# Kernel optimization log

Hardware: AMD Instinct MI355X
Metric: run time of the kernel (lower is better)

The kernel has to match this reference:

```python
import jax, jax.numpy as jnp
import numpy as np

NEG_INF = -1e6  # d2l masked_softmax mask value

def setup_inputs() -> dict:
    key = jax.random.key(0)
    ks = jax.random.split(key, 6)
    B, Lq, Lk, dq, dv, H = 8, 256, 512, 256, 256, 64
    return {
        "queries": jax.random.normal(ks[0], (B, Lq, dq), jnp.float32),
        "keys": jax.random.normal(ks[1], (B, Lk, dq), jnp.float32),
        "values": jax.random.normal(ks[2], (B, Lk, dv), jnp.float32),
        "valid_lens": jax.random.randint(ks[3], (B,), 0, Lk),
        "W_q": jax.random.normal(ks[4], (H, dq), jnp.float32) * (dq ** -0.5),
        "W_k": jax.random.normal(ks[5], (H, dq), jnp.float32) * (dq ** -0.5),
        "w_v": jax.random.normal(jax.random.fold_in(key, 7), (H,), jnp.float32) * (H ** -0.5),
    }

def reference(queries, keys, values, valid_lens, W_q, W_k, w_v):
    # Project: [B,Lq,H], [B,Lk,H]
    q = jnp.einsum('bqd,hd->bqh', queries, W_q)
    k = jnp.einsum('bkd,hd->bkh', keys, W_k)
    # Broadcast-add + tanh: [B,Lq,Lk,H]
    features = jnp.tanh(q[:, :, None, :] + k[:, None, :, :])
    # Scalar projection -> scores [B,Lq,Lk]
    scores = jnp.einsum('bqkh,h->bqk', features, w_v)
    # masked_softmax over last axis with per-batch valid_lens
    Lk = keys.shape[1]
    mask = jnp.arange(Lk)[None, None, :] < valid_lens[:, None, None]
    scores = jnp.where(mask, scores, NEG_INF)
    attn = jax.nn.softmax(scores, axis=-1)
    # dropout p=0 (inference) -> identity; bmm with values
    return jnp.einsum('bqk,bkv->bqv', attn, values)
```

## Files before the change

### kernel.cpp

```cpp
#include <hip/hip_runtime.h>
#include <hip/hip_bf16.h>
#include <hip/hip_fp16.h>
#include <stdint.h>

#define NB 8
#define LQ 256
#define LK 512
#define NH 64
#define SCALE 2.8853900817779268f
#define L2E 1.4426950408889634f

#define QP_OFF   0
#define KP_OFF   131072
#define VBF_OFF  393216
#define PML_OFF  917504

extern "C" __device__ float __ocml_exp2_f32(float);
static __device__ __forceinline__ float fexp2(float x) {
#if __has_builtin(__builtin_amdgcn_exp2f)
  return __builtin_amdgcn_exp2f(x);
#else
  return __ocml_exp2_f32(x);
#endif
}
static __device__ __forceinline__ float frcp(float x) {
  return __builtin_amdgcn_rcpf(x);
}
static __device__ __forceinline__ uint16_t f2bf(float f) {
  uint32_t u = __float_as_uint(f);
  uint32_t r = (u + 0x7FFFu + ((u >> 16) & 1u)) >> 16;
  return (uint16_t)r;
}

typedef const __attribute__((address_space(1))) void* gas_ptr;
typedef __attribute__((address_space(3))) void* las_ptr;
static __device__ __forceinline__ void gload16(const void* g, void* l) {
  __builtin_amdgcn_global_load_lds((gas_ptr)g, (las_ptr)l, 16, 0, 0);
}

__global__ __launch_bounds__(256) void proj_kernel(
    const float* __restrict__ queries, const float* __restrict__ keys,
    const float* __restrict__ values,
    const float* __restrict__ Wq, const float* __restrict__ Wk,
    float* __restrict__ qp, float* __restrict__ kp, uint16_t* __restrict__ vbf)
{
  __shared__ float Wt[256][36];
  const int blk = blockIdx.x;
  const int t = threadIdx.x;

  if (blk >= 384) {
    int base = (blk - 384) * 16384 + t * 4;
#pragma unroll
    for (int it = 0; it < 16; ++it) {
      int idx = base + it * 1024;
      float4 v = *(const float4*)(values + idx);
      uint32_t lo = (uint32_t)f2bf(v.x) | ((uint32_t)f2bf(v.y) << 16);
      uint32_t hi = (uint32_t)f2bf(v.z) | ((uint32_t)f2bf(v.w) << 16);
      uint2 pk = {lo, hi};
      *(uint2*)(vbf + idx) = pk;
    }
    return;
  }

  const bool isQ = (blk < 128);
  const int sub = isQ ? blk : (blk - 128);
  const int tile = sub >> 1;
  const int hh = (sub & 1) * 32;
  const int rowbase = tile * 32;
  const float* __restrict__ X = isQ ? queries : keys;
  const float* __restrict__ W = isQ ? Wq : Wk;
  float* __restrict__ P = isQ ? qp : kp;

#pragma unroll 4
  for (int it = 0; it < 32; ++it) {
    Wt[t][it] = W[(hh + it) * 256 + t];
  }
  __syncthreads();

  const int ty = t >> 4;
  const int tx = t & 15;
  float acc[2][2];
  acc[0][0] = acc[0][1] = acc[1][0] = acc[1][1] = 0.f;

  const float* xr0 = X + (rowbase + ty * 2 + 0) * 256;
  const float* xr1 = X + (rowbase + ty * 2 + 1) * 256;

#pragma unroll 4
  for (int d4 = 0; d4 < 64; ++d4) {
    int d = d4 * 4;
    float4 x0 = *(const float4*)(xr0 + d);
    float4 x1 = *(const float4*)(xr1 + d);
    float2 w0 = *(float2*)&Wt[d + 0][tx * 2];
    float2 w1 = *(float2*)&Wt[d + 1][tx * 2];
    float2 w2 = *(float2*)&Wt[d + 2][tx * 2];
    float2 w3 = *(float2*)&Wt[d + 3][tx * 2];
#define STEP(XC, WD) \
    acc[0][0] = fmaf(x0.XC, WD.x, acc[0][0]); acc[0][1] = fmaf(x0.XC, WD.y, acc[0][1]); \
    acc[1][0] = fmaf(x1.XC, WD.x, acc[1][0]); acc[1][1] = fmaf(x1.XC, WD.y, acc[1][1]);
    STEP(x, w0) STEP(y, w1) STEP(z, w2) STEP(w, w3)
#undef STEP
  }

#pragma unroll
  for (int i = 0; i < 2; ++i) {
    int row = rowbase + ty * 2 + i;
#pragma unroll
    for (int j = 0; j < 2; ++j) {
      int h = hh + tx * 2 + j;
      P[row * 64 + h] = acc[i][j] * SCALE;
    }
  }
}

__global__ __launch_bounds__(256) void attn_kernel(
    const float* __restrict__ qp, const float* __restrict__ kp,
    const uint16_t* __restrict__ vbf, const float* __restrict__ w_v,
    const int* __restrict__ valid_lens, float* __restrict__ out,
    float* __restrict__ pml, __half* __restrict__ pacc, int nsplit)
{
  __shared__ float kTs[2][32][64];
  __shared__ uint16_t Vs[2][32][256];
  __shared__ float q_s[4][2][64];
  __shared__ float w_s[64];
  __shared__ float p_s[4][2][32];

  const int t = threadIdx.x;
  const int lane = t & 63;
  const int w = t >> 6;
  const int r2 = lane >> 5;
  const int kj = lane & 31;
  const int wg = blockIdx.x;
  const int b = wg & 7;
  const int qg = (wg >> 3) & 31;
  const int kh = wg >> 8;
  const int row = b * LQ + qg * 8 + w * 2 + r2;

  const int vl = valid_lens[b];
  const int n = (vl > 0) ? vl : LK;
  const int span = LK / nsplit;
  const int kstart = kh * span;
  int cnt = n - kstart;
  if (cnt > span) cnt = span;
  const int ntiles = (cnt > 0) ? ((cnt + 31) >> 5) : 0;

  if (ntiles == 0) {
    if (kj == 0) {
      pml[(row * nsplit + kh) * 2 + 0] = -1e30f;
      pml[(row * nsplit + kh) * 2 + 1] = 0.f;
    }
    return;
  }

  {
    const float2* qsrc = (const float2*)(qp + (size_t)(b * LQ + qg * 8) * 64);
    ((float2*)q_s)[t] = qsrc[t];
    if (t < 64) w_s[t] = w_v[t];
  }

  float W1 = 0.f;
#pragma unroll
  for (int g = 0; g < 16; ++g) {
    float4 wf = *(const float4*)(w_v + g * 4);
    W1 += (wf.x + wf.y) + (wf.z + wf.w);
  }

  const float* kpb = kp + (size_t)(b * LK) * 64;
  const char* vbc = (const char*)(vbf + (size_t)b * LK * 256);

#define STAGE(BUF, K0) do { \
    int i0 = w * 2; \
    int kjr0 = i0 * 4 + (lane >> 4); \
    int cph = lane & 15; \
    gload16(kpb + (size_t)((K0) + kjr0) * 64 + (cph ^ (kjr0 & 7)) * 4, \
            &kTs[BUF][i0 * 4][0]); \
    int kjr1 = kjr0 + 4; \
    gload16(kpb + (size_t)((K0) + kjr1) * 64 + (cph ^ (kjr1 & 7)) * 4, \
            &kTs[BUF][i0 * 4 + 4][0]); \
    const char* vsrc = vbc + (size_t)(K0) * 512 + (size_t)w * 4096 + lane * 16; \
    gload16(vsrc + 0 * 1024, &Vs[BUF][w * 8 + 0][0]); \
    gload16(vsrc + 1 * 1024, &Vs[BUF][w * 8 + 2][0]); \
    gload16(vsrc + 2 * 1024, &Vs[BUF][w * 8 + 4][0]); \
    gload16(vsrc + 3 * 1024, &Vs[BUF][w * 8 + 6][0]); \
  } while (0)

  float m = -1e30f, l = 0.f;
  float acc[8];
#pragma unroll
  for (int i = 0; i < 8; ++i) acc[i] = 0.f;

  STAGE(0, kstart);
  __syncthreads();

  for (int tt = 0; tt < ntiles; ++tt) {
    const int cur = tt & 1;
    const int k0 = kstart + tt * 32;
    if (tt + 1 < ntiles) STAGE(cur ^ 1, k0 + 32);

    float r0 = 0.f, r1 = 0.f, r2a = 0.f, r3 = 0.f;
#pragma unroll
    for (int g = 0; g < 16; ++g) {
      float4 kf = *(const float4*)&kTs[cur][kj][((g ^ (kj & 7)) << 2)];
      float4 qf = *(const float4*)&q_s[w][r2][g * 4];
      float4 wf = *(const float4*)&w_s[g * 4];
      r0  = fmaf(wf.x, frcp(1.f + fexp2(qf.x + kf.x)), r0);
      r1  = fmaf(wf.y, frcp(1.f + fexp2(qf.y + kf.y)), r1);
      r2a = fmaf(wf.z, frcp(1.f + fexp2(qf.z + kf.z)), r2a);
      r3  = fmaf(wf.w, frcp(1.f + fexp2(qf.w + kf.w)), r3);
    }
    float racc = (r0 + r1) + (r2a + r3);

    float score;
    int kg = k0 + kj;
    if (vl == 0)      score = 0.f;
    else if (kg < n)  score = fmaf(-2.f, racc, W1);
    else              score = -1e30f;

    float mt = score;
#pragma unroll
    for (int s = 16; s; s >>= 1) mt = fmaxf(mt, __shfl_xor(mt, s, 64));
    float mnew = fmaxf(m, mt);
    float alpha = fexp2((m - mnew) * L2E);
    float p = fexp2((score - mnew) * L2E);
    m = mnew;
    float S = p;
#pragma unroll
    for (int s = 16; s; s >>= 1) S += __shfl_xor(S, s, 64);
    l = l * alpha + S;
    p_s[w][r2][kj] = p;

#pragma unroll
    for (int i = 0; i < 8; ++i) acc[i] *= alpha;
#pragma unroll
    for (int kj4 = 0; kj4 < 8; ++kj4) {
      float4 pf = *(const float4*)&p_s[w][r2][kj4 * 4];
#pragma unroll
      for (int jj = 0; jj < 4; ++jj) {
        int kk = kj4 * 4 + jj;
        uint4 vv = *(const uint4*)&Vs[cur][kk][kj * 8];
        float pj = (jj == 0) ? pf.x : (jj == 1) ? pf.y : (jj == 2) ? pf.z : pf.w;
        float f0 = __uint_as_float(vv.x << 16);
        float f1 = __uint_as_float(vv.x & 0xFFFF0000u);
        float f2 = __uint_as_float(vv.y << 16);
        float f3 = __uint_as_float(vv.y & 0xFFFF0000u);
        float f4 = __uint_as_float(vv.z << 16);
        float f5 = __uint_as_float(vv.z & 0xFFFF0000u);
        float f6 = __uint_as_float(vv.w << 16);
        float f7 = __uint_as_float(vv.w & 0xFFFF0000u);
        acc[0] = fmaf(pj, f0, acc[0]);
        acc[1] = fmaf(pj, f1, acc[1]);
        acc[2] = fmaf(pj, f2, acc[2]);
        acc[3] = fmaf(pj, f3, acc[3]);
        acc[4] = fmaf(pj, f4, acc[4]);
        acc[5] = fmaf(pj, f5, acc[5]);
        acc[6] = fmaf(pj, f6, acc[6]);
        acc[7] = fmaf(pj, f7, acc[7]);
      }
    }
    __syncthreads();
  }
#undef STAGE

  if (nsplit == 1) {
    float inv = 1.f / l;
    float4 o0 = {acc[0] * inv, acc[1] * inv, acc[2] * inv, acc[3] * inv};
    float4 o1 = {acc[4] * inv, acc[5] * inv, acc[6] * inv, acc[7] * inv};
    float* op = out + (size_t)row * 256 + kj * 8;
    *(float4*)(op + 0) = o0;
    *(float4*)(op + 4) = o1;
  } else {
    if (kj == 0) {
      pml[(row * nsplit + kh) * 2 + 0] = m;
      pml[(row * nsplit + kh) * 2 + 1] = l;
    }
    __half2 h0 = __floats2half2_rn(acc[0], acc[1]);
    __half2 h1 = __floats2half2_rn(acc[2], acc[3]);
    __half2 h2 = __floats2half2_rn(acc[4], acc[5]);
    __half2 h3 = __floats2half2_rn(acc[6], acc[7]);
    uint4 pk = {*(uint32_t*)&h0, *(uint32_t*)&h1, *(uint32_t*)&h2, *(uint32_t*)&h3};
    *(uint4*)(pacc + ((size_t)(row * nsplit + kh)) * 256 + kj * 8) = pk;
  }
}

__global__ __launch_bounds__(256) void merge_kernel(
    const float* __restrict__ pml, const __half* __restrict__ pacc,
    float* __restrict__ out, int nsplit)
{
  const int t = threadIdx.x;
  const int row = blockIdx.x * 8 + (t >> 5);
  const int d8 = t & 31;

  float ms = -1e30f;
  for (int kh = 0; kh < nsplit; ++kh)
    ms = fmaxf(ms, pml[(row * nsplit + kh) * 2]);

  float L = 0.f;
  float o[8];
#pragma unroll
  for (int i = 0; i < 8; ++i) o[i] = 0.f;

  for (int kh = 0; kh < nsplit; ++kh) {
    float mk = pml[(row * nsplit + kh) * 2 + 0];
    float lk = pml[(row * nsplit + kh) * 2 + 1];
    if (lk > 0.f) {
      float e = fexp2((mk - ms) * L2E);
      L += e * lk;
      uint4 pk = *(const uint4*)(pacc + ((size_t)(row * nsplit + kh)) * 256 + d8 * 8);
      __half2 h0 = *(__half2*)&pk.x, h1 = *(__half2*)&pk.y;
      __half2 h2 = *(__half2*)&pk.z, h3 = *(__half2*)&pk.w;
      float2 f0 = __half22float2(h0), f1 = __half22float2(h1);
      float2 f2 = __half22float2(h2), f3 = __half22float2(h3);
      o[0] = fmaf(e, f0.x, o[0]); o[1] = fmaf(e, f0.y, o[1]);
      o[2] = fmaf(e, f1.x, o[2]); o[3] = fmaf(e, f1.y, o[3]);
      o[4] = fmaf(e, f2.x, o[4]); o[5] = fmaf(e, f2.y, o[5]);
      o[6] = fmaf(e, f3.x, o[6]); o[7] = fmaf(e, f3.y, o[7]);
    }
  }
  float inv = 1.f / L;
  float4 o0 = {o[0] * inv, o[1] * inv, o[2] * inv, o[3] * inv};
  float4 o1 = {o[4] * inv, o[5] * inv, o[6] * inv, o[7] * inv};
  float* op = out + (size_t)row * 256 + d8 * 8;
  *(float4*)(op + 0) = o0;
  *(float4*)(op + 4) = o1;
}

extern "C" void kernel_launch(void* const* d_in, const int* in_sizes, int n_in,
                              void* d_out, int out_size, void* d_ws, size_t ws_size,
                              hipStream_t stream) {
  const float* queries    = (const float*)d_in[0];
  const float* keys       = (const float*)d_in[1];
  const float* values     = (const float*)d_in[2];
  const int*   valid_lens = (const int*)d_in[3];
  const float* Wq         = (const float*)d_in[4];
  const float* Wk         = (const float*)d_in[5];
  const float* w_v        = (const float*)d_in[6];
  float* out = (float*)d_out;

  float* ws = (float*)d_ws;
  float* qp  = ws + QP_OFF;
  float* kp  = ws + KP_OFF;
  uint16_t* vbf = (uint16_t*)(ws + VBF_OFF);
  float* pml = ws + PML_OFF;

  int nsplit;
  if      (ws_size >= (size_t)PML_OFF * 4 + 2048u * 4 * 8 + 2048u * 4 * 512) nsplit = 4;
  else if (ws_size >= (size_t)PML_OFF * 4 + 2048u * 2 * 8 + 2048u * 2 * 512) nsplit = 2;
  else nsplit = 1;
  __half* pacc = (__half*)(pml + (size_t)2048 * nsplit * 2);

  hipLaunchKernelGGL(proj_kernel, dim3(448), dim3(256), 0, stream,
                     queries, keys, values, Wq, Wk, qp, kp, vbf);
  hipLaunchKernelGGL(attn_kernel, dim3(nsplit * 256), dim3(256), 0, stream,
                     qp, kp, vbf, w_v, valid_lens, out, pml, pacc, nsplit);
  if (nsplit > 1) {
    hipLaunchKernelGGL(merge_kernel, dim3(256), dim3(256), 0, stream,
                       pml, pacc, out, nsplit);
  }
}
```

Before: 45.70 us.

## Hold q in registers, split PV accumulation by key half across lanes, shrink proj tiles

The projection kernel now gives each thread one row and uses twice as many blocks, which raises parallelism in the first launch. In the attention kernel, each lane keeps its query row in 64 registers instead of reading it from shared memory, and reads w_v straight from global memory. The PV accumulation is re-partitioned so each half-wave handles half of the key tile for both rows, and the halves are combined with cross-lane shuffles at the end. This halves the LDS V reads per lane, at the cost of more registers (64 for q plus 16 accumulators) and possibly lower occupancy.

```diff
diff --git a/kernel.cpp b/kernel.cpp
--- a/kernel.cpp
+++ b/kernel.cpp
@@ -48,8 +48,8 @@
   const int blk = blockIdx.x;
   const int t = threadIdx.x;
 
-  if (blk >= 384) {
-    int base = (blk - 384) * 16384 + t * 4;
+  if (blk >= 768) {
+    int base = (blk - 768) * 16384 + t * 4;
 #pragma unroll
     for (int it = 0; it < 16; ++it) {
       int idx = base + it * 1024;
@@ -62,11 +62,11 @@
     return;
   }
 
-  const bool isQ = (blk < 128);
-  const int sub = isQ ? blk : (blk - 128);
+  const bool isQ = (blk < 256);
+  const int sub = isQ ? blk : (blk - 256);
   const int tile = sub >> 1;
   const int hh = (sub & 1) * 32;
-  const int rowbase = tile * 32;
+  const int rowbase = tile * 16;
   const float* __restrict__ X = isQ ? queries : keys;
   const float* __restrict__ W = isQ ? Wq : Wk;
   float* __restrict__ P = isQ ? qp : kp;
@@ -79,36 +79,29 @@
 
   const int ty = t >> 4;
   const int tx = t & 15;
-  float acc[2][2];
-  acc[0][0] = acc[0][1] = acc[1][0] = acc[1][1] = 0.f;
-
-  const float* xr0 = X + (rowbase + ty * 2 + 0) * 256;
-  const float* xr1 = X + (rowbase + ty * 2 + 1) * 256;
+  float a0 = 0.f, a1 = 0.f;
+
+  const float* xr0 = X + (rowbase + ty) * 256;
 
 #pragma unroll 4
   for (int d4 = 0; d4 < 64; ++d4) {
     int d = d4 * 4;
     float4 x0 = *(const float4*)(xr0 + d);
-    float4 x1 = *(const float4*)(xr1 + d);
     float2 w0 = *(float2*)&Wt[d + 0][tx * 2];
     float2 w1 = *(float2*)&Wt[d + 1][tx * 2];
     float2 w2 = *(float2*)&Wt[d + 2][tx * 2];
     float2 w3 = *(float2*)&Wt[d + 3][tx * 2];
-#define STEP(XC, WD) \
-    acc[0][0] = fmaf(x0.XC, WD.x, acc[0][0]); acc[0][1] = fmaf(x0.XC, WD.y, acc[0][1]); \
-    acc[1][0] = fmaf(x1.XC, WD.x, acc[1][0]); acc[1][1] = fmaf(x1.XC, WD.y, acc[1][1]);
-    STEP(x, w0) STEP(y, w1) STEP(z, w2) STEP(w, w3)
-#undef STEP
-  }
-
-#pragma unroll
-  for (int i = 0; i < 2; ++i) {
-    int row = rowbase + ty * 2 + i;
-#pragma unroll
-    for (int j = 0; j < 2; ++j) {
-      int h = hh + tx * 2 + j;
-      P[row * 64 + h] = acc[i][j] * SCALE;
-    }
+    a0 = fmaf(x0.x, w0.x, a0); a1 = fmaf(x0.x, w0.y, a1);
+    a0 = fmaf(x0.y, w1.x, a0); a1 = fmaf(x0.y, w1.y, a1);
+    a0 = fmaf(x0.z, w2.x, a0); a1 = fmaf(x0.z, w2.y, a1);
+    a0 = fmaf(x0.w, w3.x, a0); a1 = fmaf(x0.w, w3.y, a1);
+  }
+
+  {
+    int row = rowbase + ty;
+    int h = hh + tx * 2;
+    P[row * 64 + h + 0] = a0 * SCALE;
+    P[row * 64 + h + 1] = a1 * SCALE;
   }
 }
 
@@ -120,8 +113,6 @@
 {
   __shared__ float kTs[2][32][64];
   __shared__ uint16_t Vs[2][32][256];
-  __shared__ float q_s[4][2][64];
-  __shared__ float w_s[64];
   __shared__ float p_s[4][2][32];
 
   const int t = threadIdx.x;
@@ -151,17 +142,22 @@
     return;
   }
 
-  {
-    const float2* qsrc = (const float2*)(qp + (size_t)(b * LQ + qg * 8) * 64);
-    ((float2*)q_s)[t] = qsrc[t];
-    if (t < 64) w_s[t] = w_v[t];
-  }
-
   float W1 = 0.f;
 #pragma unroll
   for (int g = 0; g < 16; ++g) {
     float4 wf = *(const float4*)(w_v + g * 4);
     W1 += (wf.x + wf.y) + (wf.z + wf.w);
+  }
+
+  float qv[64];
+  {
+    const float* qrow = qp + (size_t)row * 64;
+#pragma unroll
+    for (int i = 0; i < 16; ++i) {
+      float4 v = *(const float4*)(qrow + i * 4);
+      qv[i * 4 + 0] = v.x; qv[i * 4 + 1] = v.y;
+      qv[i * 4 + 2] = v.z; qv[i * 4 + 3] = v.w;
+    }
   }
 
   const float* kpb = kp + (size_t)(b * LK) * 64;
@@ -184,9 +180,9 @@
   } while (0)
 
   float m = -1e30f, l = 0.f;
-  float acc[8];
-#pragma unroll
-  for (int i = 0; i < 8; ++i) acc[i] = 0.f;
+  float acc[16];
+#pragma unroll
+  for (int i = 0; i < 16; ++i) acc[i] = 0.f;
 
   STAGE(0, kstart);
   __syncthreads();
@@ -200,12 +196,11 @@
 #pragma unroll
     for (int g = 0; g < 16; ++g) {
       float4 kf = *(const float4*)&kTs[cur][kj][((g ^ (kj & 7)) << 2)];
-      float4 qf = *(const float4*)&q_s[w][r2][g * 4];
-      float4 wf = *(const float4*)&w_s[g * 4];
-      r0  = fmaf(wf.x, frcp(1.f + fexp2(qf.x + kf.x)), r0);
-      r1  = fmaf(wf.y, frcp(1.f + fexp2(qf.y + kf.y)), r1);
-      r2a = fmaf(wf.z, frcp(1.f + fexp2(qf.z + kf.z)), r2a);
-      r3  = fmaf(wf.w, frcp(1.f + fexp2(qf.w + kf.w)), r3);
+      float4 wf = *(const float4*)(w_v + g * 4);
+      r0  = fmaf(wf.x, frcp(1.f + fexp2(qv[g * 4 + 0] + kf.x)), r0);
+      r1  = fmaf(wf.y, frcp(1.f + fexp2(qv[g * 4 + 1] + kf.y)), r1);
+      r2a = fmaf(wf.z, frcp(1.f + fexp2(qv[g * 4 + 2] + kf.z)), r2a);
+      r3  = fmaf(wf.w, frcp(1.f + fexp2(qv[g * 4 + 3] + kf.w)), r3);
     }
     float racc = (r0 + r1) + (r2a + r3);
 
@@ -228,16 +223,25 @@
     l = l * alpha + S;
     p_s[w][r2][kj] = p;
 
-#pragma unroll
-    for (int i = 0; i < 8; ++i) acc[i] *= alpha;
-#pragma unroll
-    for (int kj4 = 0; kj4 < 8; ++kj4) {
-      float4 pf = *(const float4*)&p_s[w][r2][kj4 * 4];
+    float alpha_x = __shfl_xor(alpha, 32, 64);
+    float a0 = (r2 == 0) ? alpha : alpha_x;
+    float a1 = (r2 == 0) ? alpha_x : alpha;
+#pragma unroll
+    for (int i = 0; i < 8; ++i)  acc[i] *= a0;
+#pragma unroll
+    for (int i = 8; i < 16; ++i) acc[i] *= a1;
+
+    const int c = kj;
+#pragma unroll
+    for (int i4 = 0; i4 < 4; ++i4) {
+      float4 p0 = *(const float4*)&p_s[w][0][r2 * 16 + i4 * 4];
+      float4 p1 = *(const float4*)&p_s[w][1][r2 * 16 + i4 * 4];
 #pragma unroll
       for (int jj = 0; jj < 4; ++jj) {
-        int kk = kj4 * 4 + jj;
-        uint4 vv = *(const uint4*)&Vs[cur][kk][kj * 8];
-        float pj = (jj == 0) ? pf.x : (jj == 1) ? pf.y : (jj == 2) ? pf.z : pf.w;
+        int kk = r2 * 16 + i4 * 4 + jj;
+        uint4 vv = *(const uint4*)&Vs[cur][kk][c * 8];
+        float pj0 = (jj == 0) ? p0.x : (jj == 1) ? p0.y : (jj == 2) ? p0.z : p0.w;
+        float pj1 = (jj == 0) ? p1.x : (jj == 1) ? p1.y : (jj == 2) ? p1.z : p1.w;
         float f0 = __uint_as_float(vv.x << 16);
         float f1 = __uint_as_float(vv.x & 0xFFFF0000u);
         float f2 = __uint_as_float(vv.y << 16);
@@ -246,24 +250,28 @@
         float f5 = __uint_as_float(vv.z & 0xFFFF0000u);
         float f6 = __uint_as_float(vv.w << 16);
         float f7 = __uint_as_float(vv.w & 0xFFFF0000u);
-        acc[0] = fmaf(pj, f0, acc[0]);
-        acc[1] = fmaf(pj, f1, acc[1]);
-        acc[2] = fmaf(pj, f2, acc[2]);
-        acc[3] = fmaf(pj, f3, acc[3]);
-        acc[4] = fmaf(pj, f4, acc[4]);
-        acc[5] = fmaf(pj, f5, acc[5]);
-        acc[6] = fmaf(pj, f6, acc[6]);
-        acc[7] = fmaf(pj, f7, acc[7]);
+        acc[0] = fmaf(pj0, f0, acc[0]);   acc[8]  = fmaf(pj1, f0, acc[8]);
+        acc[1] = fmaf(pj0, f1, acc[1]);   acc[9]  = fmaf(pj1, f1, acc[9]);
+        acc[2] = fmaf(pj0, f2, acc[2]);   acc[10] = fmaf(pj1, f2, acc[10]);
+        acc[3] = fmaf(pj0, f3, acc[3]);   acc[11] = fmaf(pj1, f3, acc[11]);
+        acc[4] = fmaf(pj0, f4, acc[4]);   acc[12] = fmaf(pj1, f4, acc[12]);
+        acc[5] = fmaf(pj0, f5, acc[5]);   acc[13] = fmaf(pj1, f5, acc[13]);
+        acc[6] = fmaf(pj0, f6, acc[6]);   acc[14] = fmaf(pj1, f6, acc[14]);
+        acc[7] = fmaf(pj0, f7, acc[7]);   acc[15] = fmaf(pj1, f7, acc[15]);
       }
     }
     __syncthreads();
   }
 #undef STAGE
 
+#pragma unroll
+  for (int i = 0; i < 16; ++i) acc[i] += __shfl_xor(acc[i], 32, 64);
+
+  const float* accr = acc + r2 * 8;
   if (nsplit == 1) {
     float inv = 1.f / l;
-    float4 o0 = {acc[0] * inv, acc[1] * inv, acc[2] * inv, acc[3] * inv};
-    float4 o1 = {acc[4] * inv, acc[5] * inv, acc[6] * inv, acc[7] * inv};
+    float4 o0 = {accr[0] * inv, accr[1] * inv, accr[2] * inv, accr[3] * inv};
+    float4 o1 = {accr[4] * inv, accr[5] * inv, accr[6] * inv, accr[7] * inv};
     float* op = out + (size_t)row * 256 + kj * 8;
     *(float4*)(op + 0) = o0;
     *(float4*)(op + 4) = o1;
@@ -272,10 +280,10 @@
       pml[(row * nsplit + kh) * 2 + 0] = m;
       pml[(row * nsplit + kh) * 2 + 1] = l;
     }
-    __half2 h0 = __floats2half2_rn(acc[0], acc[1]);
-    __half2 h1 = __floats2half2_rn(acc[2], acc[3]);
-    __half2 h2 = __floats2half2_rn(acc[4], acc[5]);
-    __half2 h3 = __floats2half2_rn(acc[6], acc[7]);
+    __half2 h0 = __floats2half2_rn(accr[0], accr[1]);
+    __half2 h1 = __floats2half2_rn(accr[2], accr[3]);
+    __half2 h2 = __floats2half2_rn(accr[4], accr[5]);
+    __half2 h3 = __floats2half2_rn(accr[6], accr[7]);
     uint4 pk = {*(uint32_t*)&h0, *(uint32_t*)&h1, *(uint32_t*)&h2, *(uint32_t*)&h3};
     *(uint4*)(pacc + ((size_t)(row * nsplit + kh)) * 256 + kj * 8) = pk;
   }
@@ -347,7 +355,7 @@
   else nsplit = 1;
   __half* pacc = (__half*)(pml + (size_t)2048 * nsplit * 2);
 
-  hipLaunchKernelGGL(proj_kernel, dim3(448), dim3(256), 0, stream,
+  hipLaunchKernelGGL(proj_kernel, dim3(832), dim3(256), 0, stream,
                      queries, keys, values, Wq, Wk, qp, kp, vbf);
   hipLaunchKernelGGL(attn_kernel, dim3(nsplit * 256), dim3(256), 0, stream,
                      qp, kp, vbf, w_v, valid_lens, out, pml, pacc, nsplit);
```

Measured after the change: 44.21 us. -3.3%, faster.
